# Kernel optimization log

Hardware: AMD Instinct MI355X
Metric: run time of the kernel (lower is better)

## Reference

```python
import jax, jax.numpy as jnp
import numpy as np

N = 20000
E = 80000
D = 1024


def setup_inputs() -> dict:
    key = jax.random.key(0)
    ks = jax.random.split(key, 12)
    s1 = 1.0 / np.sqrt(2 * D)
    s2 = 1.0 / np.sqrt(D)
    return {
        "x": jax.random.normal(ks[0], (N, D), dtype=jnp.float32),
        "edge_index": jax.random.randint(ks[1], (2, E), 0, N, dtype=jnp.int64),
        "edge_attr": jax.random.normal(ks[2], (E, D), dtype=jnp.float32),
        "W1a": jax.random.uniform(ks[3], (2 * D, D), jnp.float32, -s1, s1),
        "b1a": jax.random.uniform(ks[4], (D,), jnp.float32, -s1, s1),
        "W1b": jax.random.uniform(ks[5], (D, D), jnp.float32, -s2, s2),
        "b1b": jax.random.uniform(ks[6], (D,), jnp.float32, -s2, s2),
        "W2a": jax.random.uniform(ks[7], (2 * D, D), jnp.float32, -s1, s1),
        "b2a": jax.random.uniform(ks[8], (D,), jnp.float32, -s1, s1),
        "W2b": jax.random.uniform(ks[9], (D, D), jnp.float32, -s2, s2),
        "b2b": jax.random.uniform(ks[10], (D,), jnp.float32, -s2, s2),
    }


def reference(x, edge_index, edge_attr, W1a, b1a, W1b, b1b, W2a, b2a, W2b, b2b):
    row, col = edge_index[0], edge_index[1]
    # gather source node features, concat edge features: [E, 2D]
    h = jnp.concatenate([x[row], edge_attr], axis=1)
    # node_mlp_1: Lin(2D,D) -> ReLU -> Lin(D,D)
    h = jax.nn.relu(h @ W1a + b1a) @ W1b + b1b  # [E, D]
    # scatter_mean over destination nodes (dim_size = N); empty segments -> 0
    sums = jax.ops.segment_sum(h, col, num_segments=N)  # [N, D]
    counts = jax.ops.segment_sum(jnp.ones((h.shape[0], 1), h.dtype), col, num_segments=N)
    mean = sums / jnp.maximum(counts, 1.0)
    # (scatter_max is computed in the torch code but its result is unused)
    out = jnp.concatenate([x, mean], axis=1)  # [N, 2D]
    # node_mlp_2
    return jax.nn.relu(out @ W2a + b2a) @ W2b + b2b  # [N, D]
```

## Files before the change

kernel.cpp:

```cpp
#include <hip/hip_runtime.h>
#include <stdint.h>

#define NN 20000
#define NE 80000
#define DD 1024

typedef __bf16 bf16x8 __attribute__((ext_vector_type(8)));
typedef float f32x4 __attribute__((ext_vector_type(4)));
typedef unsigned short u16;
typedef unsigned int u32;

__device__ __forceinline__ float bf2f(u16 v) { return __uint_as_float(((u32)v) << 16); }
__device__ __forceinline__ u16 f2bf(float f) { return (u16)((__float_as_uint(f) + 0x8000u) >> 16); }

__device__ __forceinline__ void lds_dma16(const u16* g, u16* l) {
  __builtin_amdgcn_global_load_lds((const __attribute__((address_space(1))) u32*)g,
                                   (__attribute__((address_space(3))) u32*)l, 16, 0, 0);
}

__global__ void detect_stride_k(const int* __restrict__ ei, int* flag) {
  if (threadIdx.x == 0) {
    int nz = 0;
    for (int i = 1; i < 128; i += 2) nz |= ei[i];
    *flag = (nz == 0) ? 2 : 1;
  }
}

__global__ void transpose_cvt_k(const float* __restrict__ in, u16* __restrict__ out) {
  __shared__ float tile[32][33];
  int bx = blockIdx.x * 32, by = blockIdx.y * 32;
  int tx = threadIdx.x & 31, ty = threadIdx.x >> 5;
#pragma unroll
  for (int s = 0; s < 4; s++)
    tile[ty + s * 8][tx] = in[(size_t)(by + ty + s * 8) * DD + bx + tx];
  __syncthreads();
#pragma unroll
  for (int s = 0; s < 4; s++)
    out[(size_t)(bx + ty + s * 8) * DD + by + tx] = f2bf(tile[tx][ty + s * 8]);
}

__global__ void cvt_bf16_k(const float4* __restrict__ in, ushort4* __restrict__ out, int n4) {
  int i = blockIdx.x * 256 + threadIdx.x;
  if (i < n4) {
    float4 f = in[i];
    ushort4 o;
    o.x = f2bf(f.x); o.y = f2bf(f.y); o.z = f2bf(f.z); o.w = f2bf(f.w);
    out[i] = o;
  }
}

__global__ void count_edges_k(const int* __restrict__ ei, const int* __restrict__ sflag,
                              int* __restrict__ cnt) {
  int e = blockIdx.x * 256 + threadIdx.x;
  if (e < NE) {
    int s = *sflag;
    atomicAdd(&cnt[ei[(size_t)s * (NE + e)]], 1);
  }
}

__global__ __launch_bounds__(1024) void scan_k(const int* __restrict__ cnt,
                                               int* __restrict__ rowptr, int* __restrict__ ofs) {
  __shared__ int part[1024];
  int t = threadIdx.x;
  int base = t * 20;
  int loc[20];
  int s = 0;
#pragma unroll
  for (int i = 0; i < 20; i++) {
    int v = (base + i < NN) ? cnt[base + i] : 0;
    loc[i] = s; s += v;
  }
  part[t] = s;
  __syncthreads();
  for (int d = 1; d < 1024; d <<= 1) {
    int v = (t >= d) ? part[t - d] : 0;
    __syncthreads();
    part[t] += v;
    __syncthreads();
  }
  int excl = (t > 0) ? part[t - 1] : 0;
#pragma unroll
  for (int i = 0; i < 20; i++)
    if (base + i < NN) { rowptr[base + i] = excl + loc[i]; ofs[base + i] = excl + loc[i]; }
  if (t == 1023) rowptr[NN] = part[1023];
}

__global__ void scatter_k(const int* __restrict__ ei, const int* __restrict__ sflag,
                          int* __restrict__ ofs, int* __restrict__ perm) {
  int e = blockIdx.x * 256 + threadIdx.x;
  if (e < NE) {
    int s = *sflag;
    int c = ei[(size_t)s * (NE + e)];
    perm[atomicAdd(&ofs[c], 1)] = e;
  }
}

__global__ void seg_mean_k(const u16* __restrict__ h, const int* __restrict__ rowptr,
                           const int* __restrict__ perm, u16* __restrict__ sbar) {
  int n = blockIdx.x, t = threadIdx.x;
  int beg = rowptr[n], end = rowptr[n + 1];
  float a0 = 0, a1 = 0, a2 = 0, a3 = 0;
  for (int i = beg; i < end; i++) {
    int e = perm[i];
    ushort4 v = *(const ushort4*)(h + (size_t)e * DD + t * 4);
    a0 += bf2f(v.x); a1 += bf2f(v.y); a2 += bf2f(v.z); a3 += bf2f(v.w);
  }
  float inv = (end > beg) ? 1.0f / (float)(end - beg) : 0.0f;
  ushort4 o;
  o.x = f2bf(a0 * inv); o.y = f2bf(a1 * inv); o.z = f2bf(a2 * inv); o.w = f2bf(a3 * inv);
  *(ushort4*)(sbar + (size_t)n * DD + t * 4) = o;
}

template <int EPI, int NSRC>
__global__ __launch_bounds__(256, 3) void gemm_k(
    const u16* __restrict__ A0, const u16* __restrict__ A1,
    const u16* __restrict__ B0, const u16* __restrict__ B1, int M,
    const float* __restrict__ bias, float* __restrict__ Cout, u16* __restrict__ Cbf,
    const u16* __restrict__ Pg, u16* __restrict__ Hout,
    const int* __restrict__ eidx, const int* __restrict__ sflag,
    const int* __restrict__ cnt) {
  __shared__ __align__(16) u16 As[3][128 * 32];
  __shared__ __align__(16) u16 Bs[3][128 * 32];

  const int tid = threadIdx.x;
  const int lane = tid & 63;
  const int wv = tid >> 6;
  const int wm = wv >> 1, wn = wv & 1;

  const int nwg = gridDim.x;
  const int cpx = nwg >> 3;
  const int bid = blockIdx.x;
  const int l = (bid & 7) * cpx + (bid >> 3);
  const int nblk = l & 7, mblk = l >> 3;

  const int lrow = lane & 15, kq = lane >> 4;

  int ss = 1;
  if constexpr (EPI == 1) {
    ss = *sflag;
    asm volatile("s_waitcnt vmcnt(0)" ::: "memory");
  }

  size_t a_goff[2], b_goff[2];
  int lseg[2];
#pragma unroll
  for (int r = 0; r < 2; r++) {
    int p = (wv * 2 + r) * 64 + lane;
    int row = p >> 2, c = p & 3;
    int kc = c ^ ((row >> 1) & 3);
    a_goff[r] = (size_t)min(mblk * 128 + row, M - 1) * DD + kc * 8;
    b_goff[r] = (size_t)(nblk * 128 + row) * DD + kc * 8;
    lseg[r] = (wv * 2 + r) * 512;
  }

  int a_fo[4], b_fo[4];
#pragma unroll
  for (int i = 0; i < 4; i++) {
    int m = wm * 64 + i * 16 + lrow;
    a_fo[i] = (m * 4 + (kq ^ ((m >> 1) & 3))) * 8;
    int n = wn * 64 + i * 16 + lrow;
    b_fo[i] = (n * 4 + (kq ^ ((n >> 1) & 3))) * 8;
  }

  f32x4 acc[4][4] = {};

  const int NK = NSRC * (DD / 32);

  auto stage = [&](int b, int step) {
    const u16* Ag = A0;
    const u16* Bg = B0;
    if constexpr (NSRC == 2) {
      if (step >= DD / 32) { Ag = A1; Bg = B1; }
    }
    size_t ko = (size_t)(step & (DD / 32 - 1)) * 32;
#pragma unroll
    for (int r = 0; r < 2; r++) {
      lds_dma16(Ag + a_goff[r] + ko, &As[b][lseg[r]]);
      lds_dma16(Bg + b_goff[r] + ko, &Bs[b][lseg[r]]);
    }
  };

  auto compute = [&](int cb) {
    bf16x8 af[4], bf[4];
#pragma unroll
    for (int i = 0; i < 4; i++) {
      af[i] = *(const bf16x8*)&As[cb][a_fo[i]];
      bf[i] = *(const bf16x8*)&Bs[cb][b_fo[i]];
    }
    __builtin_amdgcn_s_setprio(1);
#pragma unroll
    for (int i = 0; i < 4; i++)
#pragma unroll
      for (int j = 0; j < 4; j++)
        acc[i][j] = __builtin_amdgcn_mfma_f32_16x16x32_bf16(af[i], bf[j], acc[i][j], 0, 0, 0);
    __builtin_amdgcn_s_setprio(0);
  };

  stage(0, 0);
  stage(1, 1);
  stage(2, 2);

  int cur = 0;
  for (int t = 0; t + 3 < NK; ++t) {
    asm volatile("s_waitcnt vmcnt(8)" ::: "memory");
    __builtin_amdgcn_s_barrier();
    asm volatile("" ::: "memory");
    compute(cur);
    asm volatile("" ::: "memory");
    __builtin_amdgcn_s_barrier();
    stage(cur, t + 3);
    cur = (cur == 2) ? 0 : cur + 1;
  }
  asm volatile("s_waitcnt vmcnt(8)" ::: "memory");
  __builtin_amdgcn_s_barrier();
  asm volatile("" ::: "memory");
  compute(cur);
  cur = (cur == 2) ? 0 : cur + 1;
  asm volatile("s_waitcnt vmcnt(4)" ::: "memory");
  __builtin_amdgcn_s_barrier();
  asm volatile("" ::: "memory");
  compute(cur);
  cur = (cur == 2) ? 0 : cur + 1;
  asm volatile("s_waitcnt vmcnt(0)" ::: "memory");
  __builtin_amdgcn_s_barrier();
  asm volatile("" ::: "memory");
  compute(cur);

#pragma unroll
  for (int i = 0; i < 4; i++) {
#pragma unroll
    for (int r = 0; r < 4; r++) {
      int grow = mblk * 128 + wm * 64 + i * 16 + kq * 4 + r;
      if (grow >= M) continue;
      int erow = 0;
      if constexpr (EPI == 1) erow = eidx[(size_t)ss * grow];
#pragma unroll
      for (int j = 0; j < 4; j++) {
        int gcol = nblk * 128 + wn * 64 + j * 16 + lrow;
        float v = acc[i][j][r];
        if constexpr (EPI == 0) {
          Cout[(size_t)grow * DD + gcol] = v + bias[gcol];
        } else if constexpr (EPI == 1) {
          float z = fmaxf(v + bf2f(Pg[(size_t)erow * DD + gcol]), 0.0f);
          Hout[(size_t)grow * DD + gcol] = f2bf(z);
        } else if constexpr (EPI == 2) {
          float b = (cnt[grow] > 0) ? bias[gcol] : 0.0f;
          Cbf[(size_t)grow * DD + gcol] = f2bf(v + b);
        } else if constexpr (EPI == 3) {
          Cbf[(size_t)grow * DD + gcol] = f2bf(fmaxf(v + bias[gcol], 0.0f));
        } else {
          Cbf[(size_t)grow * DD + gcol] = f2bf(v + bias[gcol]);
        }
      }
    }
  }
}

extern "C" void kernel_launch(void* const* d_in, const int* in_sizes, int n_in,
                              void* d_out, int out_size, void* d_ws, size_t ws_size,
                              hipStream_t stream) {
  const float* x   = (const float*)d_in[0];
  const int*   ei  = (const int*)d_in[1];
  const float* ea  = (const float*)d_in[2];
  const float* W1a = (const float*)d_in[3];
  const float* b1a = (const float*)d_in[4];
  const float* W1b = (const float*)d_in[5];
  const float* b1b = (const float*)d_in[6];
  const float* W2a = (const float*)d_in[7];
  const float* b2a = (const float*)d_in[8];
  const float* W2b = (const float*)d_in[9];
  const float* b2b = (const float*)d_in[10];
  float* out = (float*)d_out;

  char* ws = (char*)d_ws;
  size_t off = 0;
  const size_t WSZ = (size_t)DD * DD;
  u16* W1aT_t = (u16*)(ws + off); off += WSZ * 2;
  u16* W1aT_b = (u16*)(ws + off); off += WSZ * 2;
  u16* W1bT   = (u16*)(ws + off); off += WSZ * 2;
  u16* W2aT_t = (u16*)(ws + off); off += WSZ * 2;
  u16* W2aT_b = (u16*)(ws + off); off += WSZ * 2;
  u16* W2bT   = (u16*)(ws + off); off += WSZ * 2;
  u16* xb   = (u16*)(ws + off); off += (size_t)NN * DD * 2;
  u16* eb   = (u16*)(ws + off); off += (size_t)NE * DD * 2;
  u16* bufP = (u16*)(ws + off); off += (size_t)NN * DD * 2;
  u16* bufM = (u16*)(ws + off); off += (size_t)NN * DD * 2;
  u16* h    = (u16*)(ws + off); off += (size_t)NE * DD * 2;
  int* cnt    = (int*)(ws + off); off += (size_t)NN * 4;
  int* rowptr = (int*)(ws + off); off += (size_t)(NN + 1) * 4;
  int* ofs    = (int*)(ws + off); off += (size_t)NN * 4;
  int* perm   = (int*)(ws + off); off += (size_t)NE * 4;
  int* sflag  = (int*)(ws + off); off += 256;
  if (ws_size < off) return;

  dim3 tb(256);
  dim3 tg(32, 32);
  transpose_cvt_k<<<tg, tb, 0, stream>>>(W1a, W1aT_t);
  transpose_cvt_k<<<tg, tb, 0, stream>>>(W1a + WSZ, W1aT_b);
  transpose_cvt_k<<<tg, tb, 0, stream>>>(W1b, W1bT);
  transpose_cvt_k<<<tg, tb, 0, stream>>>(W2a, W2aT_t);
  transpose_cvt_k<<<tg, tb, 0, stream>>>(W2a + WSZ, W2aT_b);
  transpose_cvt_k<<<tg, tb, 0, stream>>>(W2b, W2bT);

  cvt_bf16_k<<<NN * DD / 4 / 256, tb, 0, stream>>>((const float4*)x, (ushort4*)xb, NN * DD / 4);
  cvt_bf16_k<<<NE * DD / 4 / 256, tb, 0, stream>>>((const float4*)ea, (ushort4*)eb, NE * DD / 4);

  detect_stride_k<<<1, 64, 0, stream>>>(ei, sflag);
  hipMemsetAsync(cnt, 0, (size_t)NN * 4, stream);
  count_edges_k<<<(NE + 255) / 256, tb, 0, stream>>>(ei, sflag, cnt);
  scan_k<<<1, 1024, 0, stream>>>(cnt, rowptr, ofs);
  scatter_k<<<(NE + 255) / 256, tb, 0, stream>>>(ei, sflag, ofs, perm);

  const int nmbN = (NN + 127) / 128;
  const int nmbE = NE / 128;
  dim3 gN(8 * nmbN);
  dim3 gE(8 * nmbE);

  gemm_k<4, 1><<<gN, tb, 0, stream>>>(xb, nullptr, W1aT_t, nullptr, NN,
                                      b1a, nullptr, bufP, nullptr, nullptr,
                                      nullptr, nullptr, nullptr);
  gemm_k<1, 1><<<gE, tb, 0, stream>>>(eb, nullptr, W1aT_b, nullptr, NE,
                                      nullptr, nullptr, nullptr, bufP, h,
                                      ei, sflag, nullptr);
  seg_mean_k<<<NN, tb, 0, stream>>>(h, rowptr, perm, bufP);
  gemm_k<2, 1><<<gN, tb, 0, stream>>>(bufP, nullptr, W1bT, nullptr, NN,
                                      b1b, nullptr, bufM, nullptr, nullptr,
                                      nullptr, nullptr, cnt);
  gemm_k<3, 2><<<gN, tb, 0, stream>>>(xb, bufM, W2aT_t, W2aT_b, NN,
                                      b2a, nullptr, bufP, nullptr, nullptr,
                                      nullptr, nullptr, nullptr);
  gemm_k<0, 1><<<gN, tb, 0, stream>>>(bufP, nullptr, W2bT, nullptr, NN,
                                      b2b, out, nullptr, nullptr, nullptr,
                                      nullptr, nullptr, nullptr);
}
```

Measured before the change: 1.226 ms.

## Enlarge GEMM tiles to 256x256 with 512 threads and 4-slot pipeline

```diff
diff --git a/kernel.cpp b/kernel.cpp
--- a/kernel.cpp
+++ b/kernel.cpp
@@ -112,26 +112,27 @@
 }
 
 template <int EPI, int NSRC>
-__global__ __launch_bounds__(256, 3) void gemm_k(
+__global__ __launch_bounds__(512, 2) void gemm_k(
     const u16* __restrict__ A0, const u16* __restrict__ A1,
     const u16* __restrict__ B0, const u16* __restrict__ B1, int M,
     const float* __restrict__ bias, float* __restrict__ Cout, u16* __restrict__ Cbf,
     const u16* __restrict__ Pg, u16* __restrict__ Hout,
     const int* __restrict__ eidx, const int* __restrict__ sflag,
     const int* __restrict__ cnt) {
-  __shared__ __align__(16) u16 As[3][128 * 32];
-  __shared__ __align__(16) u16 Bs[3][128 * 32];
+  __shared__ __align__(16) u16 As[4][256 * 32];
+  __shared__ __align__(16) u16 Bs[4][256 * 32];
 
   const int tid = threadIdx.x;
   const int lane = tid & 63;
   const int wv = tid >> 6;
-  const int wm = wv >> 1, wn = wv & 1;
+  const int wm = wv >> 2, wn = wv & 3;
 
   const int nwg = gridDim.x;
-  const int cpx = nwg >> 3;
-  const int bid = blockIdx.x;
-  const int l = (bid & 7) * cpx + (bid >> 3);
-  const int nblk = l & 7, mblk = l >> 3;
+  const int q = nwg >> 3, r8 = nwg & 7;
+  const int orig = blockIdx.x;
+  const int xcd = orig & 7, wg = orig >> 3;
+  const int l = (xcd < r8 ? xcd * (q + 1) : r8 * (q + 1) + (xcd - r8) * q) + wg;
+  const int nblk = l & 3, mblk = l >> 2;
 
   const int lrow = lane & 15, kq = lane >> 4;
 
@@ -148,95 +149,95 @@
     int p = (wv * 2 + r) * 64 + lane;
     int row = p >> 2, c = p & 3;
     int kc = c ^ ((row >> 1) & 3);
-    a_goff[r] = (size_t)min(mblk * 128 + row, M - 1) * DD + kc * 8;
-    b_goff[r] = (size_t)(nblk * 128 + row) * DD + kc * 8;
+    a_goff[r] = (size_t)min(mblk * 256 + row, M - 1) * DD + kc * 8;
+    b_goff[r] = (size_t)(nblk * 256 + row) * DD + kc * 8;
     lseg[r] = (wv * 2 + r) * 512;
   }
 
-  int a_fo[4], b_fo[4];
-#pragma unroll
-  for (int i = 0; i < 4; i++) {
-    int m = wm * 64 + i * 16 + lrow;
+  int a_fo[8], b_fo[4];
+#pragma unroll
+  for (int i = 0; i < 8; i++) {
+    int m = wm * 128 + i * 16 + lrow;
     a_fo[i] = (m * 4 + (kq ^ ((m >> 1) & 3))) * 8;
-    int n = wn * 64 + i * 16 + lrow;
-    b_fo[i] = (n * 4 + (kq ^ ((n >> 1) & 3))) * 8;
-  }
-
-  f32x4 acc[4][4] = {};
+  }
+#pragma unroll
+  for (int j = 0; j < 4; j++) {
+    int n = wn * 64 + j * 16 + lrow;
+    b_fo[j] = (n * 4 + (kq ^ ((n >> 1) & 3))) * 8;
+  }
+
+  f32x4 acc[8][4] = {};
 
   const int NK = NSRC * (DD / 32);
 
-  auto stage = [&](int b, int step) {
+  auto stage = [&](int H) {
     const u16* Ag = A0;
     const u16* Bg = B0;
     if constexpr (NSRC == 2) {
-      if (step >= DD / 32) { Ag = A1; Bg = B1; }
+      if (H >= DD / 32) { Ag = A1; Bg = B1; }
     }
-    size_t ko = (size_t)(step & (DD / 32 - 1)) * 32;
+    int slot = H & 3;
+    size_t ko = (size_t)(H & (DD / 32 - 1)) * 32;
 #pragma unroll
     for (int r = 0; r < 2; r++) {
-      lds_dma16(Ag + a_goff[r] + ko, &As[b][lseg[r]]);
-      lds_dma16(Bg + b_goff[r] + ko, &Bs[b][lseg[r]]);
+      lds_dma16(Ag + a_goff[r] + ko, &As[slot][lseg[r]]);
+      lds_dma16(Bg + b_goff[r] + ko, &Bs[slot][lseg[r]]);
     }
   };
 
-  auto compute = [&](int cb) {
-    bf16x8 af[4], bf[4];
-#pragma unroll
-    for (int i = 0; i < 4; i++) {
-      af[i] = *(const bf16x8*)&As[cb][a_fo[i]];
-      bf[i] = *(const bf16x8*)&Bs[cb][b_fo[i]];
-    }
+  auto compute = [&](int slot) {
+    bf16x8 af[8], bfr[4];
+#pragma unroll
+    for (int i = 0; i < 8; i++) af[i] = *(const bf16x8*)&As[slot][a_fo[i]];
+#pragma unroll
+    for (int j = 0; j < 4; j++) bfr[j] = *(const bf16x8*)&Bs[slot][b_fo[j]];
     __builtin_amdgcn_s_setprio(1);
 #pragma unroll
-    for (int i = 0; i < 4; i++)
+    for (int i = 0; i < 8; i++)
 #pragma unroll
       for (int j = 0; j < 4; j++)
-        acc[i][j] = __builtin_amdgcn_mfma_f32_16x16x32_bf16(af[i], bf[j], acc[i][j], 0, 0, 0);
+        acc[i][j] = __builtin_amdgcn_mfma_f32_16x16x32_bf16(af[i], bfr[j], acc[i][j], 0, 0, 0);
     __builtin_amdgcn_s_setprio(0);
   };
 
-  stage(0, 0);
-  stage(1, 1);
-  stage(2, 2);
-
-  int cur = 0;
-  for (int t = 0; t + 3 < NK; ++t) {
+  stage(0);
+  stage(1);
+  stage(2);
+
+  for (int j = 0; j < NK - 3; ++j) {
     asm volatile("s_waitcnt vmcnt(8)" ::: "memory");
     __builtin_amdgcn_s_barrier();
     asm volatile("" ::: "memory");
-    compute(cur);
+    stage(j + 3);
+    compute(j & 3);
     asm volatile("" ::: "memory");
-    __builtin_amdgcn_s_barrier();
-    stage(cur, t + 3);
-    cur = (cur == 2) ? 0 : cur + 1;
   }
   asm volatile("s_waitcnt vmcnt(8)" ::: "memory");
   __builtin_amdgcn_s_barrier();
   asm volatile("" ::: "memory");
-  compute(cur);
-  cur = (cur == 2) ? 0 : cur + 1;
+  compute((NK - 3) & 3);
+  asm volatile("" ::: "memory");
   asm volatile("s_waitcnt vmcnt(4)" ::: "memory");
   __builtin_amdgcn_s_barrier();
   asm volatile("" ::: "memory");
-  compute(cur);
-  cur = (cur == 2) ? 0 : cur + 1;
+  compute((NK - 2) & 3);
+  asm volatile("" ::: "memory");
   asm volatile("s_waitcnt vmcnt(0)" ::: "memory");
   __builtin_amdgcn_s_barrier();
   asm volatile("" ::: "memory");
-  compute(cur);
-
-#pragma unroll
-  for (int i = 0; i < 4; i++) {
+  compute((NK - 1) & 3);
+
+#pragma unroll
+  for (int i = 0; i < 8; i++) {
 #pragma unroll
     for (int r = 0; r < 4; r++) {
-      int grow = mblk * 128 + wm * 64 + i * 16 + kq * 4 + r;
+      int grow = mblk * 256 + wm * 128 + i * 16 + kq * 4 + r;
       if (grow >= M) continue;
       int erow = 0;
       if constexpr (EPI == 1) erow = eidx[(size_t)ss * grow];
 #pragma unroll
       for (int j = 0; j < 4; j++) {
-        int gcol = nblk * 128 + wn * 64 + j * 16 + lrow;
+        int gcol = nblk * 256 + wn * 64 + j * 16 + lrow;
         float v = acc[i][j][r];
         if constexpr (EPI == 0) {
           Cout[(size_t)grow * DD + gcol] = v + bias[gcol];
@@ -294,6 +295,7 @@
   if (ws_size < off) return;
 
   dim3 tb(256);
+  dim3 tb5(512);
   dim3 tg(32, 32);
   transpose_cvt_k<<<tg, tb, 0, stream>>>(W1a, W1aT_t);
   transpose_cvt_k<<<tg, tb, 0, stream>>>(W1a + WSZ, W1aT_b);
@@ -311,25 +313,25 @@
   scan_k<<<1, 1024, 0, stream>>>(cnt, rowptr, ofs);
   scatter_k<<<(NE + 255) / 256, tb, 0, stream>>>(ei, sflag, ofs, perm);
 
-  const int nmbN = (NN + 127) / 128;
-  const int nmbE = NE / 128;
-  dim3 gN(8 * nmbN);
-  dim3 gE(8 * nmbE);
-
-  gemm_k<4, 1><<<gN, tb, 0, stream>>>(xb, nullptr, W1aT_t, nullptr, NN,
-                                      b1a, nullptr, bufP, nullptr, nullptr,
-                                      nullptr, nullptr, nullptr);
-  gemm_k<1, 1><<<gE, tb, 0, stream>>>(eb, nullptr, W1aT_b, nullptr, NE,
-                                      nullptr, nullptr, nullptr, bufP, h,
-                                      ei, sflag, nullptr);
+  const int nmbN = (NN + 255) / 256;
+  const int nmbE = (NE + 255) / 256;
+  dim3 gN(4 * nmbN);
+  dim3 gE(4 * nmbE);
+
+  gemm_k<4, 1><<<gN, tb5, 0, stream>>>(xb, nullptr, W1aT_t, nullptr, NN,
+                                       b1a, nullptr, bufP, nullptr, nullptr,
+                                       nullptr, nullptr, nullptr);
+  gemm_k<1, 1><<<gE, tb5, 0, stream>>>(eb, nullptr, W1aT_b, nullptr, NE,
+                                       nullptr, nullptr, nullptr, bufP, h,
+                                       ei, sflag, nullptr);
   seg_mean_k<<<NN, tb, 0, stream>>>(h, rowptr, perm, bufP);
-  gemm_k<2, 1><<<gN, tb, 0, stream>>>(bufP, nullptr, W1bT, nullptr, NN,
-                                      b1b, nullptr, bufM, nullptr, nullptr,
-                                      nullptr, nullptr, cnt);
-  gemm_k<3, 2><<<gN, tb, 0, stream>>>(xb, bufM, W2aT_t, W2aT_b, NN,
-                                      b2a, nullptr, bufP, nullptr, nullptr,
-                                      nullptr, nullptr, nullptr);
-  gemm_k<0, 1><<<gN, tb, 0, stream>>>(bufP, nullptr, W2bT, nullptr, NN,
-                                      b2b, out, nullptr, nullptr, nullptr,
-                                      nullptr, nullptr, nullptr);
-}
+  gemm_k<2, 1><<<gN, tb5, 0, stream>>>(bufP, nullptr, W1bT, nullptr, NN,
+                                       b1b, nullptr, bufM, nullptr, nullptr,
+                                       nullptr, nullptr, cnt);
+  gemm_k<3, 2><<<gN, tb5, 0, stream>>>(xb, bufM, W2aT_t, W2aT_b, NN,
+                                       b2a, nullptr, bufP, nullptr, nullptr,
+                                       nullptr, nullptr, nullptr);
+  gemm_k<0, 1><<<gN, tb5, 0, stream>>>(bufP, nullptr, W2bT, nullptr, NN,
+                                       b2b, out, nullptr, nullptr, nullptr,
+                                       nullptr, nullptr, nullptr);
+}
```

After: 1.434 ms. +17.0%, slower.
